# Kernel optimization log

Measured on AMD Instinct MI355X. Metric: run time of the kernel, lower is better.

## Reference

```python
import jax, jax.numpy as jnp
import numpy as np


def setup_inputs() -> dict:
    key = jax.random.key(0)
    ks = jax.random.split(key, 7)
    B, d_model, Hs, Ws = 16, 384, 64, 64
    state_dim, d_inner = 64, 768
    L = Hs * Ws
    return {
        "x": jax.random.normal(ks[0], (B, d_model, L), jnp.float32),
        "w_bcdt": jax.random.normal(ks[1], (3 * state_dim, d_model), jnp.float32) * 0.05,
        "w_dw": jax.random.normal(ks[2], (3 * state_dim, 1, 3, 3), jnp.float32) * 0.3,
        "w_hz": jax.random.normal(ks[3], (2 * d_inner, d_model), jnp.float32) * 0.05,
        "w_out": jax.random.normal(ks[4], (d_model, d_inner), jnp.float32) * 0.05,
        "a_param": jax.random.uniform(ks[5], (state_dim,), jnp.float32, 1.0, 16.0),
        "d_param": jnp.ones((1,), jnp.float32),
        "H": Hs,
        "W": Ws,
    }


def reference(x, w_bcdt, w_dw, w_hz, w_out, a_param, d_param, H, W):
    batch, d_model, L = x.shape
    state_dim = a_param.shape[0]
    d_inner = w_out.shape[1]
    conv_dim = 3 * state_dim

    # 1x1 conv projection: (B, 3*state_dim, L)
    bc_dt = jnp.einsum("od,bdl->bol", w_bcdt, x)
    # depthwise 3x3 conv on the (H, W) spatial grid
    bc_dt = bc_dt.reshape(batch, conv_dim, H, W)
    bc_dt = jax.lax.conv_general_dilated(
        bc_dt, w_dw, window_strides=(1, 1), padding=((1, 1), (1, 1)),
        dimension_numbers=("NCHW", "OIHW", "NCHW"),
        feature_group_count=conv_dim,
    ).reshape(batch, conv_dim, L)

    Bm, Cm, dt = jnp.split(bc_dt, 3, axis=1)  # each (B, state_dim, L)
    A = jax.nn.softmax(dt + a_param[None, :, None], axis=-1)
    AB = A * Bm  # (B, state_dim, L)

    # state aggregation: (B, d_model, state_dim)
    h = jnp.einsum("bdl,bsl->bds", x, AB)
    hz = jnp.einsum("od,bds->bos", w_hz, h)  # (B, 2*d_inner, state_dim)
    h_i, z = jnp.split(hz, 2, axis=1)
    h = jnp.einsum("od,bds->bos", w_out, h_i * jax.nn.silu(z) + h_i * d_param)

    # broadcast state back to tokens: (B, d_model, L)
    y = jnp.einsum("bds,bsl->bdl", h, Cm).reshape(batch, d_model, H, W)
    return y, h
```

## Files before the change

kernel.cpp:

```cpp
#include <hip/hip_runtime.h>
#include <hip/hip_bf16.h>

#define BATCH 16
#define DMODEL 384
#define LTOK 4096
#define SDIM 64
#define C3 192
#define DINNER 768

typedef __attribute__((ext_vector_type(8))) short short8;
typedef __attribute__((ext_vector_type(4))) float f32x4;

__device__ __forceinline__ short f2bf(float f) {
    unsigned u = __builtin_bit_cast(unsigned, f);
    u += 0x7fffu + ((u >> 16) & 1u);
    return (short)(u >> 16);
}
__device__ __forceinline__ float bf2f(short s) {
    return __builtin_bit_cast(float, ((unsigned)(unsigned short)s) << 16);
}

template<int BN, int NF, bool AF32, bool BF32, int CMODE>
__global__ __launch_bounds__(256) void gemm_bf16(
    const void* __restrict__ Ap, const void* __restrict__ Bp, void* __restrict__ Cp,
    int M, int N, int K, long sA, long sB, long sC, int nTilesN, int splitK)
{
    const int b = blockIdx.z;
    const int ntile  = blockIdx.x % nTilesN;
    const int kchunk = blockIdx.x / nTilesN;
    const int row0 = blockIdx.y << 6;
    const int col0 = ntile * BN;
    const int kPer = K / splitK;
    const int kBeg = kchunk * kPer, kEnd = kBeg + kPer;

    __shared__ short As[64][40];
    __shared__ short Bs[BN][40];

    const int t = threadIdx.x;
    const int wid = t >> 6, lane = t & 63;
    const int lr = lane & 15;
    const int lk = (lane >> 4) << 3;

    f32x4 acc[4][NF];
#pragma unroll
    for (int i = 0; i < 4; i++)
#pragma unroll
        for (int j = 0; j < NF; j++)
#pragma unroll
            for (int r = 0; r < 4; r++) acc[i][j][r] = 0.f;

    for (int kt = kBeg; kt < kEnd; kt += 32) {
        {
            const int arow = t >> 2, akb = (t & 3) << 3;
            if constexpr (AF32) {
                const float* s = (const float*)Ap + b * sA + (long)(row0 + arow) * K + kt + akb;
                short8 v;
#pragma unroll
                for (int j = 0; j < 8; j++) v[j] = f2bf(s[j]);
                *(short8*)&As[arow][akb] = v;
            } else {
                const short* s = (const short*)Ap + b * sA + (long)(row0 + arow) * K + kt + akb;
                *(short8*)&As[arow][akb] = *(const short8*)s;
            }
        }
#pragma unroll
        for (int rr = 0; rr < BN / 64; rr++) {
            const int u = t + rr * 256;
            const int brow = u >> 2, bkb = (u & 3) << 3;
            if constexpr (BF32) {
                const float* s = (const float*)Bp + b * sB + (long)(col0 + brow) * K + kt + bkb;
                short8 v;
#pragma unroll
                for (int j = 0; j < 8; j++) v[j] = f2bf(s[j]);
                *(short8*)&Bs[brow][bkb] = v;
            } else {
                const short* s = (const short*)Bp + b * sB + (long)(col0 + brow) * K + kt + bkb;
                *(short8*)&Bs[brow][bkb] = *(const short8*)s;
            }
        }
        __syncthreads();

        short8 af[4], bfr[NF];
#pragma unroll
        for (int mi = 0; mi < 4; mi++) af[mi] = *(const short8*)&As[mi * 16 + lr][lk];
#pragma unroll
        for (int ni = 0; ni < NF; ni++) bfr[ni] = *(const short8*)&Bs[wid * (BN / 4) + ni * 16 + lr][lk];
#pragma unroll
        for (int mi = 0; mi < 4; mi++)
#pragma unroll
            for (int ni = 0; ni < NF; ni++)
                acc[mi][ni] = __builtin_amdgcn_mfma_f32_16x16x32_bf16(af[mi], bfr[ni], acc[mi][ni], 0, 0, 0);
        __syncthreads();
    }

#pragma unroll
    for (int mi = 0; mi < 4; mi++)
#pragma unroll
        for (int ni = 0; ni < NF; ni++)
#pragma unroll
            for (int r = 0; r < 4; r++) {
                const long row = row0 + mi * 16 + ((lane >> 4) << 2) + r;
                const long col = col0 + wid * (BN / 4) + ni * 16 + lr;
                if constexpr (CMODE == 1)      atomicAdd((float*)Cp + b * sC + row * N + col, acc[mi][ni][r]);
                else if constexpr (CMODE == 2) *((short*)Cp + b * sC + row * N + col) = f2bf(acc[mi][ni][r]);
                else                           *((float*)Cp + b * sC + row * N + col) = acc[mi][ni][r];
            }
}

__global__ __launch_bounds__(256) void transpose_x(const float* __restrict__ x, short* __restrict__ xbT)
{
    const int b = blockIdx.z;
    const int l0 = blockIdx.x << 6, d0 = blockIdx.y << 6;
    __shared__ float tl[64][65];
    const int t = threadIdx.x, c = t & 63, r0 = t >> 6;
    const float* ip = x + ((long)b * DMODEL + d0) * LTOK + l0;
    for (int d = r0; d < 64; d += 4) tl[d][c] = ip[(long)d * LTOK + c];
    __syncthreads();
    short* op = xbT + ((long)b * LTOK + l0) * DMODEL + d0;
    for (int l = r0; l < 64; l += 4) op[(long)l * DMODEL + c] = f2bf(tl[c][l]);
}

__global__ __launch_bounds__(256) void conv_softmax_ab(
    const short* __restrict__ bcdt, const float* __restrict__ w_dw, short* __restrict__ AB)
{
    const int b = blockIdx.x >> 6, s = blockIdx.x & 63;
    __shared__ float pB[4096];
    __shared__ float pD[4096];
    __shared__ float wB[9], wD[9];
    __shared__ float redm[4], reds[4];
    const int t = threadIdx.x;

    const short* srcB = bcdt + ((long)b * C3 + s) * 4096;
    const short* srcD = bcdt + ((long)b * C3 + 128 + s) * 4096;
#pragma unroll
    for (int j = 0; j < 2; j++) {
        const int o = (t + j * 256) * 8;
        short8 vb = *(const short8*)(srcB + o);
        short8 vd = *(const short8*)(srcD + o);
#pragma unroll
        for (int e = 0; e < 8; e++) { pB[o + e] = bf2f(vb[e]); pD[o + e] = bf2f(vd[e]); }
    }
    if (t < 9) { wB[t] = w_dw[s * 9 + t]; wD[t] = w_dw[(128 + s) * 9 + t]; }
    __syncthreads();

    float v[16];
    float mx = -1e30f;
#pragma unroll
    for (int i = 0; i < 16; i++) {
        const int l = t + i * 256, y = l >> 6, x = l & 63;
        float sacc = 0.f;
#pragma unroll
        for (int dy = -1; dy <= 1; dy++)
#pragma unroll
            for (int dx = -1; dx <= 1; dx++) {
                int yy = y + dy, xx = x + dx;
                if (yy >= 0 && yy < 64 && xx >= 0 && xx < 64)
                    sacc += pD[yy * 64 + xx] * wD[(dy + 1) * 3 + (dx + 1)];
            }
        v[i] = sacc; mx = fmaxf(mx, sacc);
    }
#pragma unroll
    for (int o = 32; o > 0; o >>= 1) mx = fmaxf(mx, __shfl_xor(mx, o));
    const int wid = t >> 6;
    if ((t & 63) == 0) redm[wid] = mx;
    __syncthreads();
    mx = fmaxf(fmaxf(redm[0], redm[1]), fmaxf(redm[2], redm[3]));

    float sum = 0.f;
#pragma unroll
    for (int i = 0; i < 16; i++) { v[i] = __expf(v[i] - mx); sum += v[i]; }
#pragma unroll
    for (int o = 32; o > 0; o >>= 1) sum += __shfl_xor(sum, o);
    if ((t & 63) == 0) reds[wid] = sum;
    __syncthreads();
    sum = reds[0] + reds[1] + reds[2] + reds[3];
    const float inv = 1.0f / sum;

    short* ab = AB + ((long)b * SDIM + s) * (long)LTOK;
#pragma unroll
    for (int i = 0; i < 16; i++) {
        const int l = t + i * 256, y = l >> 6, x = l & 63;
        float uacc = 0.f;
#pragma unroll
        for (int dy = -1; dy <= 1; dy++)
#pragma unroll
            for (int dx = -1; dx <= 1; dx++) {
                int yy = y + dy, xx = x + dx;
                if (yy >= 0 && yy < 64 && xx >= 0 && xx < 64)
                    uacc += pB[yy * 64 + xx] * wB[(dy + 1) * 3 + (dx + 1)];
            }
        ab[l] = f2bf(v[i] * inv * uacc);
    }
}

__global__ __launch_bounds__(256) void dwconv_cm(
    const short* __restrict__ bcdt, const float* __restrict__ w, float* __restrict__ convCm)
{
    const int bc = blockIdx.x;
    const int b = bc >> 6, cc = bc & 63;
    __shared__ float tile[4096];
    __shared__ float wc[9];
    const short* ip = bcdt + ((long)b * C3 + 64 + cc) * 4096;
    const int t = threadIdx.x;
#pragma unroll
    for (int j = 0; j < 2; j++) {
        const int o = (t + j * 256) * 8;
        short8 vv = *(const short8*)(ip + o);
#pragma unroll
        for (int e = 0; e < 8; e++) tile[o + e] = bf2f(vv[e]);
    }
    if (t < 9) wc[t] = w[(64 + cc) * 9 + t];
    __syncthreads();
    float* op = convCm + (long)bc * 4096;
    for (int i = t; i < 4096; i += 256) {
        int y = i >> 6, x = i & 63;
        float sacc = 0.f;
#pragma unroll
        for (int dy = -1; dy <= 1; dy++)
#pragma unroll
            for (int dx = -1; dx <= 1; dx++) {
                int yy = y + dy, xx = x + dx;
                if (yy >= 0 && yy < 64 && xx >= 0 && xx < 64)
                    sacc += tile[yy * 64 + xx] * wc[(dy + 1) * 3 + (dx + 1)];
            }
        op[i] = sacc;
    }
}

__global__ __launch_bounds__(256) void transpose_cm(
    const float* __restrict__ convCm, short* __restrict__ CmT)
{
    const int b = blockIdx.y, l0 = blockIdx.x << 6;
    __shared__ float tl[64][65];
    const int t = threadIdx.x, c = t & 63, r0 = t >> 6;
    const float* ip = convCm + (long)b * SDIM * LTOK + l0;
    for (int s = r0; s < 64; s += 4) tl[s][c] = ip[(long)s * LTOK + c];
    __syncthreads();
    short* op = CmT + ((long)b * LTOK + l0) * SDIM;
    for (int l = r0; l < 64; l += 4) op[(long)l * SDIM + c] = f2bf(tl[c][l]);
}

__global__ __launch_bounds__(256) void gate_k(
    const float* __restrict__ hzT, const float* __restrict__ d_param, float* __restrict__ gT)
{
    const long i = (long)blockIdx.x * 256 + threadIdx.x;
    const long b = i / (SDIM * DINNER), r = i % (SDIM * DINNER);
    const long s = r / DINNER, o = r % DINNER;
    const float* hp = hzT + b * (SDIM * 2L * DINNER) + s * (2L * DINNER);
    const float hi = hp[o];
    const float z  = hp[DINNER + o];
    const float sil = z / (1.f + __expf(-z));
    gT[i] = hi * (sil + d_param[0]);
}

__global__ __launch_bounds__(256) void transpose_hout(
    const float* __restrict__ houtT, float* __restrict__ hout, short* __restrict__ hb)
{
    const int b = blockIdx.y, d0 = blockIdx.x << 6;
    __shared__ float tl[64][65];
    const int t = threadIdx.x, c = t & 63, r0 = t >> 6;
    const float* ip = houtT + (long)b * SDIM * DMODEL + d0;
    for (int s = r0; s < 64; s += 4) tl[s][c] = ip[(long)s * DMODEL + c];
    __syncthreads();
    float* op = hout + ((long)b * DMODEL + d0) * SDIM;
    short* ob = hb + ((long)b * DMODEL + d0) * SDIM;
    for (int d = r0; d < 64; d += 4) {
        float v = tl[c][d];
        op[(long)d * SDIM + c] = v;
        ob[(long)d * SDIM + c] = f2bf(v);
    }
}

extern "C" void kernel_launch(void* const* d_in, const int* in_sizes, int n_in,
                              void* d_out, int out_size, void* d_ws, size_t ws_size,
                              hipStream_t stream) {
    const float* x      = (const float*)d_in[0];
    const float* w_bcdt = (const float*)d_in[1];
    const float* w_dw   = (const float*)d_in[2];
    const float* w_hz   = (const float*)d_in[3];
    const float* w_out  = (const float*)d_in[4];
    const float* dparam = (const float*)d_in[6];

    char* ws = (char*)d_ws;
    short* xbT    = (short*)(ws);
    short* bcdt   = (short*)(ws + 50331648);
    short* AB     = (short*)(ws + 75497472);
    float* convCm = (float*)(ws + 83886080);
    short* CmT    = (short*)(ws + 100663296);
    float* hT     = (float*)(ws + 109051904);
    float* hzT    = (float*)(ws + 110624768);
    float* gT     = (float*)(ws + 116916224);
    float* houtT  = (float*)(ws + 120061952);
    short* hb     = (short*)(ws + 121634816);

    float* y    = (float*)d_out;
    float* hout = (float*)d_out + 25165824;

    transpose_x<<<dim3(64, 6, 16), 256, 0, stream>>>(x, xbT);

    gemm_bf16<256, 4, true, false, 2><<<dim3(16, 3, BATCH), 256, 0, stream>>>(
        w_bcdt, xbT, bcdt, C3, LTOK, DMODEL,
        0L, (long)LTOK * DMODEL, (long)C3 * LTOK, 16, 1);

    conv_softmax_ab<<<dim3(BATCH * SDIM), 256, 0, stream>>>(bcdt, w_dw, AB);

    dwconv_cm<<<dim3(BATCH * SDIM), 256, 0, stream>>>(bcdt, w_dw, convCm);

    transpose_cm<<<dim3(64, 16), 256, 0, stream>>>(convCm, CmT);

    hipMemsetAsync(hT, 0, (size_t)BATCH * SDIM * DMODEL * 4, stream);
    gemm_bf16<128, 2, false, true, 1><<<dim3(3 * 8, 1, BATCH), 256, 0, stream>>>(
        AB, x, hT, SDIM, DMODEL, LTOK,
        (long)SDIM * LTOK, (long)DMODEL * LTOK, (long)SDIM * DMODEL, 3, 8);

    gemm_bf16<128, 2, true, true, 0><<<dim3(12, 1, BATCH), 256, 0, stream>>>(
        hT, w_hz, hzT, SDIM, 2 * DINNER, DMODEL,
        (long)SDIM * DMODEL, 0L, (long)SDIM * 2 * DINNER, 12, 1);

    gate_k<<<dim3((BATCH * SDIM * DINNER) / 256), 256, 0, stream>>>(hzT, dparam, gT);

    gemm_bf16<128, 2, true, true, 0><<<dim3(3, 1, BATCH), 256, 0, stream>>>(
        gT, w_out, houtT, SDIM, DMODEL, DINNER,
        (long)SDIM * DINNER, 0L, (long)SDIM * DMODEL, 3, 1);

    transpose_hout<<<dim3(6, 16), 256, 0, stream>>>(houtT, hout, hb);

    gemm_bf16<256, 4, false, false, 0><<<dim3(16, 6, BATCH), 256, 0, stream>>>(
        hb, CmT, y, DMODEL, LTOK, SDIM,
        (long)DMODEL * SDIM, (long)LTOK * SDIM, (long)DMODEL * LTOK, 16, 1);
}
```

Before: 353.0 us.

## Fuse gate into out-projection, replace atomics with split-K reduce, batch small GEMMs

Generalizes the GEMM kernel with input and output modes. The gate (silu) is now computed while loading the A tile of the w_out GEMM, and the h output transpose is folded into that GEMM's epilogue. The split-K atomic accumulation plus memset becomes a partials buffer followed by a reduce kernel. The small per-batch GEMMs are flattened into single M=1024 GEMMs, and the first and last GEMMs are reoriented to write transposed outputs with vector stores. This removes several small kernels and intermediate round trips through memory, at the cost of 8 partial buffers and strided transposed stores.

```diff
diff --git a/kernel.cpp b/kernel.cpp
--- a/kernel.cpp
+++ b/kernel.cpp
@@ -9,6 +9,7 @@
 #define DINNER 768
 
 typedef __attribute__((ext_vector_type(8))) short short8;
+typedef __attribute__((ext_vector_type(4))) short short4v;
 typedef __attribute__((ext_vector_type(4))) float f32x4;
 
 __device__ __forceinline__ short f2bf(float f) {
@@ -20,10 +21,12 @@
     return __builtin_bit_cast(float, ((unsigned)(unsigned short)s) << 16);
 }
 
-template<int BN, int NF, bool AF32, bool BF32, int CMODE>
-__global__ __launch_bounds__(256) void gemm_bf16(
-    const void* __restrict__ Ap, const void* __restrict__ Bp, void* __restrict__ Cp,
-    int M, int N, int K, long sA, long sB, long sC, int nTilesN, int splitK)
+template<int BN, int NF, int AMODE, int BMODE, int CMODE>
+__global__ __launch_bounds__(256) void gemm_k(
+    const void* __restrict__ Ap, const void* __restrict__ Bp,
+    void* __restrict__ Cp, void* __restrict__ Cp2, const float* __restrict__ gp,
+    int M, int N, int K, int lda, int ldb,
+    long sA, long sB, long sC, int nTilesN, int splitK)
 {
     const int b = blockIdx.z;
     const int ntile  = blockIdx.x % nTilesN;
@@ -40,6 +43,7 @@
     const int wid = t >> 6, lane = t & 63;
     const int lr = lane & 15;
     const int lk = (lane >> 4) << 3;
+    const float dp = (AMODE == 2) ? gp[0] : 0.f;
 
     f32x4 acc[4][NF];
 #pragma unroll
@@ -52,29 +56,38 @@
     for (int kt = kBeg; kt < kEnd; kt += 32) {
         {
             const int arow = t >> 2, akb = (t & 3) << 3;
-            if constexpr (AF32) {
-                const float* s = (const float*)Ap + b * sA + (long)(row0 + arow) * K + kt + akb;
+            if constexpr (AMODE == 0) {
+                const short* s = (const short*)Ap + b * sA + (long)(row0 + arow) * lda + kt + akb;
+                *(short8*)&As[arow][akb] = *(const short8*)s;
+            } else if constexpr (AMODE == 1) {
+                const float* s = (const float*)Ap + b * sA + (long)(row0 + arow) * lda + kt + akb;
                 short8 v;
 #pragma unroll
                 for (int j = 0; j < 8; j++) v[j] = f2bf(s[j]);
                 *(short8*)&As[arow][akb] = v;
             } else {
-                const short* s = (const short*)Ap + b * sA + (long)(row0 + arow) * K + kt + akb;
-                *(short8*)&As[arow][akb] = *(const short8*)s;
+                const float* s = (const float*)Ap + (long)(row0 + arow) * lda + kt + akb;
+                short8 v;
+#pragma unroll
+                for (int j = 0; j < 8; j++) {
+                    float hi = s[j], z = s[DINNER + j];
+                    v[j] = f2bf(hi * (z / (1.f + __expf(-z)) + dp));
+                }
+                *(short8*)&As[arow][akb] = v;
             }
         }
 #pragma unroll
         for (int rr = 0; rr < BN / 64; rr++) {
             const int u = t + rr * 256;
             const int brow = u >> 2, bkb = (u & 3) << 3;
-            if constexpr (BF32) {
-                const float* s = (const float*)Bp + b * sB + (long)(col0 + brow) * K + kt + bkb;
+            if constexpr (BMODE == 1) {
+                const float* s = (const float*)Bp + b * sB + (long)(col0 + brow) * ldb + kt + bkb;
                 short8 v;
 #pragma unroll
                 for (int j = 0; j < 8; j++) v[j] = f2bf(s[j]);
                 *(short8*)&Bs[brow][bkb] = v;
             } else {
-                const short* s = (const short*)Bp + b * sB + (long)(col0 + brow) * K + kt + bkb;
+                const short* s = (const short*)Bp + b * sB + (long)(col0 + brow) * ldb + kt + bkb;
                 *(short8*)&Bs[brow][bkb] = *(const short8*)s;
             }
         }
@@ -93,18 +106,38 @@
         __syncthreads();
     }
 
+    const int hi4 = (lane >> 4) << 2;
 #pragma unroll
     for (int mi = 0; mi < 4; mi++)
 #pragma unroll
-        for (int ni = 0; ni < NF; ni++)
-#pragma unroll
-            for (int r = 0; r < 4; r++) {
-                const long row = row0 + mi * 16 + ((lane >> 4) << 2) + r;
-                const long col = col0 + wid * (BN / 4) + ni * 16 + lr;
-                if constexpr (CMODE == 1)      atomicAdd((float*)Cp + b * sC + row * N + col, acc[mi][ni][r]);
-                else if constexpr (CMODE == 2) *((short*)Cp + b * sC + row * N + col) = f2bf(acc[mi][ni][r]);
-                else                           *((float*)Cp + b * sC + row * N + col) = acc[mi][ni][r];
-            }
+        for (int ni = 0; ni < NF; ni++) {
+            const long row = row0 + mi * 16 + hi4;
+            const long col = col0 + wid * (BN / 4) + ni * 16 + lr;
+            if constexpr (CMODE == 0) {
+#pragma unroll
+                for (int r = 0; r < 4; r++)
+                    ((float*)Cp)[b * sC + (row + r) * N + col] = acc[mi][ni][r];
+            } else if constexpr (CMODE == 3) {
+#pragma unroll
+                for (int r = 0; r < 4; r++)
+                    ((float*)Cp)[((long)kchunk * BATCH + b) * sC + (row + r) * N + col] = acc[mi][ni][r];
+            } else if constexpr (CMODE == 4) {
+                const long bb = row >> 6, s0 = row & 63;
+                f32x4 fv = acc[mi][ni];
+                *(f32x4*)((float*)Cp + ((bb * DMODEL) + col) * SDIM + s0) = fv;
+                short4v sv;
+#pragma unroll
+                for (int r = 0; r < 4; r++) sv[r] = f2bf(acc[mi][ni][r]);
+                *(short4v*)((short*)Cp2 + ((bb * DMODEL) + col) * SDIM + s0) = sv;
+            } else if constexpr (CMODE == 5) {
+                short4v sv;
+#pragma unroll
+                for (int r = 0; r < 4; r++) sv[r] = f2bf(acc[mi][ni][r]);
+                *(short4v*)((short*)Cp + b * sC + col * (long)M + row) = sv;
+            } else {
+                *(f32x4*)((float*)Cp + b * sC + col * (long)M + row) = acc[mi][ni];
+            }
+        }
 }
 
 __global__ __launch_bounds__(256) void transpose_x(const float* __restrict__ x, short* __restrict__ xbT)
@@ -240,35 +273,22 @@
     for (int l = r0; l < 64; l += 4) op[(long)l * SDIM + c] = f2bf(tl[c][l]);
 }
 
-__global__ __launch_bounds__(256) void gate_k(
-    const float* __restrict__ hzT, const float* __restrict__ d_param, float* __restrict__ gT)
-{
-    const long i = (long)blockIdx.x * 256 + threadIdx.x;
-    const long b = i / (SDIM * DINNER), r = i % (SDIM * DINNER);
-    const long s = r / DINNER, o = r % DINNER;
-    const float* hp = hzT + b * (SDIM * 2L * DINNER) + s * (2L * DINNER);
-    const float hi = hp[o];
-    const float z  = hp[DINNER + o];
-    const float sil = z / (1.f + __expf(-z));
-    gT[i] = hi * (sil + d_param[0]);
-}
-
-__global__ __launch_bounds__(256) void transpose_hout(
-    const float* __restrict__ houtT, float* __restrict__ hout, short* __restrict__ hb)
-{
-    const int b = blockIdx.y, d0 = blockIdx.x << 6;
-    __shared__ float tl[64][65];
-    const int t = threadIdx.x, c = t & 63, r0 = t >> 6;
-    const float* ip = houtT + (long)b * SDIM * DMODEL + d0;
-    for (int s = r0; s < 64; s += 4) tl[s][c] = ip[(long)s * DMODEL + c];
-    __syncthreads();
-    float* op = hout + ((long)b * DMODEL + d0) * SDIM;
-    short* ob = hb + ((long)b * DMODEL + d0) * SDIM;
-    for (int d = r0; d < 64; d += 4) {
-        float v = tl[c][d];
-        op[(long)d * SDIM + c] = v;
-        ob[(long)d * SDIM + c] = f2bf(v);
-    }
+__global__ __launch_bounds__(256) void reduce8(
+    const float* __restrict__ part, short* __restrict__ hT)
+{
+    const long i4 = (long)blockIdx.x * 256 + threadIdx.x;
+    const long base = i4 * 4;
+    f32x4 sum = *(const f32x4*)(part + base);
+#pragma unroll
+    for (int c = 1; c < 8; c++) {
+        f32x4 v = *(const f32x4*)(part + (long)c * 393216 + base);
+#pragma unroll
+        for (int r = 0; r < 4; r++) sum[r] += v[r];
+    }
+    short4v sv;
+#pragma unroll
+    for (int r = 0; r < 4; r++) sv[r] = f2bf(sum[r]);
+    *(short4v*)(hT + base) = sv;
 }
 
 extern "C" void kernel_launch(void* const* d_in, const int* in_sizes, int n_in,
@@ -283,24 +303,24 @@
 
     char* ws = (char*)d_ws;
     short* xbT    = (short*)(ws);
+    float* part   = (float*)(ws);
+    short* hT     = (short*)(ws + 12582912);
+    float* hzT    = (float*)(ws + 13631488);
+    short* hb     = (short*)(ws + 19922944);
     short* bcdt   = (short*)(ws + 50331648);
     short* AB     = (short*)(ws + 75497472);
     float* convCm = (float*)(ws + 83886080);
     short* CmT    = (short*)(ws + 100663296);
-    float* hT     = (float*)(ws + 109051904);
-    float* hzT    = (float*)(ws + 110624768);
-    float* gT     = (float*)(ws + 116916224);
-    float* houtT  = (float*)(ws + 120061952);
-    short* hb     = (short*)(ws + 121634816);
 
     float* y    = (float*)d_out;
     float* hout = (float*)d_out + 25165824;
 
     transpose_x<<<dim3(64, 6, 16), 256, 0, stream>>>(x, xbT);
 
-    gemm_bf16<256, 4, true, false, 2><<<dim3(16, 3, BATCH), 256, 0, stream>>>(
-        w_bcdt, xbT, bcdt, C3, LTOK, DMODEL,
-        0L, (long)LTOK * DMODEL, (long)C3 * LTOK, 16, 1);
+    gemm_k<192, 3, 0, 1, 5><<<dim3(1, 64, 16), 256, 0, stream>>>(
+        xbT, w_bcdt, bcdt, nullptr, nullptr,
+        LTOK, C3, DMODEL, DMODEL, DMODEL,
+        (long)LTOK * DMODEL, 0L, (long)C3 * LTOK, 1, 1);
 
     conv_softmax_ab<<<dim3(BATCH * SDIM), 256, 0, stream>>>(bcdt, w_dw, AB);
 
@@ -308,24 +328,25 @@
 
     transpose_cm<<<dim3(64, 16), 256, 0, stream>>>(convCm, CmT);
 
-    hipMemsetAsync(hT, 0, (size_t)BATCH * SDIM * DMODEL * 4, stream);
-    gemm_bf16<128, 2, false, true, 1><<<dim3(3 * 8, 1, BATCH), 256, 0, stream>>>(
-        AB, x, hT, SDIM, DMODEL, LTOK,
+    gemm_k<128, 2, 0, 1, 3><<<dim3(3 * 8, 1, 16), 256, 0, stream>>>(
+        AB, x, part, nullptr, nullptr,
+        SDIM, DMODEL, LTOK, LTOK, LTOK,
         (long)SDIM * LTOK, (long)DMODEL * LTOK, (long)SDIM * DMODEL, 3, 8);
 
-    gemm_bf16<128, 2, true, true, 0><<<dim3(12, 1, BATCH), 256, 0, stream>>>(
-        hT, w_hz, hzT, SDIM, 2 * DINNER, DMODEL,
-        (long)SDIM * DMODEL, 0L, (long)SDIM * 2 * DINNER, 12, 1);
-
-    gate_k<<<dim3((BATCH * SDIM * DINNER) / 256), 256, 0, stream>>>(hzT, dparam, gT);
-
-    gemm_bf16<128, 2, true, true, 0><<<dim3(3, 1, BATCH), 256, 0, stream>>>(
-        gT, w_out, houtT, SDIM, DMODEL, DINNER,
-        (long)SDIM * DINNER, 0L, (long)SDIM * DMODEL, 3, 1);
-
-    transpose_hout<<<dim3(6, 16), 256, 0, stream>>>(houtT, hout, hb);
-
-    gemm_bf16<256, 4, false, false, 0><<<dim3(16, 6, BATCH), 256, 0, stream>>>(
-        hb, CmT, y, DMODEL, LTOK, SDIM,
-        (long)DMODEL * SDIM, (long)LTOK * SDIM, (long)DMODEL * LTOK, 16, 1);
-}
+    reduce8<<<dim3(384), 256, 0, stream>>>(part, hT);
+
+    gemm_k<128, 2, 0, 1, 0><<<dim3(12, 16, 1), 256, 0, stream>>>(
+        hT, w_hz, hzT, nullptr, nullptr,
+        1024, 2 * DINNER, DMODEL, DMODEL, DMODEL,
+        0L, 0L, 0L, 12, 1);
+
+    gemm_k<64, 1, 2, 1, 4><<<dim3(6, 16, 1), 256, 0, stream>>>(
+        hzT, w_out, hout, hb, dparam,
+        1024, DMODEL, DINNER, 2 * DINNER, DINNER,
+        0L, 0L, 0L, 6, 1);
+
+    gemm_k<128, 2, 0, 0, 6><<<dim3(3, 64, 16), 256, 0, stream>>>(
+        CmT, hb, y, nullptr, nullptr,
+        LTOK, DMODEL, SDIM, SDIM, SDIM,
+        (long)LTOK * SDIM, (long)DMODEL * SDIM, (long)DMODEL * LTOK, 3, 1);
+}
```

Result: no change. 352.3 us (-0.2%).
